# Optimization experiments

Measured on AMD Instinct MI355X. Metric: run time of the kernel, lower is better.

The kernel has to match this reference:

```python
import jax, jax.numpy as jnp
import numpy as np

EMB = 1024
NUM_HEADS = 16
KEY_SIZE = 64
HEAD_SIZE = 64
EPS = 1.1920929e-07  # torch RMSNorm default eps=None -> finfo(float32).eps


def setup_inputs() -> dict:
    key = jax.random.key(0)
    ks = jax.random.split(key, 6)
    B, S = 2, 2048
    qkv_out = 2 * KEY_SIZE * NUM_HEADS + HEAD_SIZE * NUM_HEADS  # 3072
    return {
        "embeddings": jax.random.normal(ks[0], (B, S, EMB), dtype=jnp.float32),
        "cos_buffer": jax.random.uniform(ks[1], (S, KEY_SIZE), dtype=jnp.float32),
        "sin_buffer": jax.random.uniform(ks[2], (S, KEY_SIZE), dtype=jnp.float32),
        "norm_weight": jnp.ones((EMB,), dtype=jnp.float32),
        "qkv_weight": jax.random.normal(ks[3], (qkv_out, EMB), dtype=jnp.float32) * (EMB ** -0.5),
        "out_weight": jax.random.normal(ks[4], (EMB, NUM_HEADS * HEAD_SIZE), dtype=jnp.float32) * ((NUM_HEADS * HEAD_SIZE) ** -0.5),
    }


def _rotate(feat, cos_b, sin_b):
    # feat: [B, H, S, key_size]; torch code: cat(second_half, first_half) (no negation)
    half = KEY_SIZE // 2
    swapped = jnp.concatenate((feat[..., half:], feat[..., :half]), axis=-1)
    return cos_b * feat + sin_b * swapped


def reference(embeddings, cos_buffer, sin_buffer, norm_weight, qkv_weight, out_weight):
    B, S, D = embeddings.shape
    # RMSNorm
    rms = jnp.sqrt(jnp.mean(embeddings * embeddings, axis=-1, keepdims=True) + EPS)
    normed = embeddings / rms * norm_weight
    # fused QKV projection (torch Linear: x @ W.T)
    qkv = normed @ qkv_weight.T  # [B, S, 3072]
    ks = KEY_SIZE * NUM_HEADS
    q = qkv[..., :ks].reshape(B, S, NUM_HEADS, KEY_SIZE).transpose(0, 2, 1, 3)
    k = qkv[..., ks:2 * ks].reshape(B, S, NUM_HEADS, KEY_SIZE).transpose(0, 2, 1, 3)
    v = qkv[..., 2 * ks:].reshape(B, S, NUM_HEADS, HEAD_SIZE).transpose(0, 2, 1, 3)
    q = _rotate(q, cos_buffer, sin_buffer)
    k = _rotate(k, cos_buffer, sin_buffer)
    # causal scaled dot product attention
    scale = 1.0 / jnp.sqrt(jnp.float32(KEY_SIZE))
    scores = jnp.einsum("bhqd,bhkd->bhqk", q, k) * scale  # [B,H,S,S]
    causal = jnp.tril(jnp.ones((S, S), dtype=bool))
    scores = jnp.where(causal, scores, jnp.float32(-jnp.inf))
    probs = jax.nn.softmax(scores, axis=-1)
    attn = jnp.einsum("bhqk,bhkd->bhqd", probs, v)  # [B,H,S,head]
    attn = attn.transpose(0, 2, 1, 3).reshape(B, S, NUM_HEADS * HEAD_SIZE)
    out = attn @ out_weight.T
    return embeddings + out
```

## Files before the change

### kernel.cpp

```cpp
#include <hip/hip_runtime.h>
#include <hip/hip_bf16.h>
#include <stdint.h>

#define EMB 1024
#define SEQ 2048
#define NB 2
#define NH 16
#define HD 64
#define QKVN 3072
#define BSROWS (NB*SEQ)

typedef __attribute__((ext_vector_type(8))) short short8;
typedef __attribute__((ext_vector_type(4))) float f32x4;
typedef __attribute__((ext_vector_type(4))) unsigned short u16x4;

__device__ __forceinline__ float bf2f(unsigned short u){
  union{uint32_t i; float f;} x; x.i = ((uint32_t)u)<<16; return x.f;
}
__device__ __forceinline__ unsigned short f2bf(float f){
  union{float f; uint32_t i;} x; x.f = f;
  return (unsigned short)((x.i + 0x7FFFu + ((x.i>>16)&1u))>>16);
}

__device__ __forceinline__ void gload_lds16(const void* g, void* l){
  __builtin_amdgcn_global_load_lds((const __attribute__((address_space(1))) void*)g,
                                   (__attribute__((address_space(3))) void*)l, 16, 0, 0);
}

__global__ __launch_bounds__(256) void k_rmsnorm(const float* __restrict__ x,
                                                 const float* __restrict__ w,
                                                 unsigned short* __restrict__ out){
  int row = blockIdx.x;
  const float4* xr = (const float4*)(x + (size_t)row*EMB);
  float4 v = xr[threadIdx.x];
  float ss = v.x*v.x + v.y*v.y + v.z*v.z + v.w*v.w;
  #pragma unroll
  for(int m=1;m<64;m<<=1) ss += __shfl_xor(ss, m, 64);
  __shared__ float red[4];
  if((threadIdx.x & 63)==0) red[threadIdx.x>>6] = ss;
  __syncthreads();
  float tot = red[0]+red[1]+red[2]+red[3];
  float rinv = rsqrtf(tot*(1.0f/EMB) + 1.1920929e-07f);
  float4 wv = ((const float4*)w)[threadIdx.x];
  u16x4 o;
  o.x = f2bf(v.x*wv.x*rinv); o.y = f2bf(v.y*wv.y*rinv);
  o.z = f2bf(v.z*wv.z*rinv); o.w = f2bf(v.w*wv.w*rinv);
  *(u16x4*)(out + (size_t)row*EMB + threadIdx.x*4) = o;
}

__global__ __launch_bounds__(256) void k_f2bf2(const float* __restrict__ a,
                                               const float* __restrict__ b,
                                               unsigned short* __restrict__ oa,
                                               unsigned short* __restrict__ ob,
                                               int na4, int nb4){
  int i = blockIdx.x*256 + threadIdx.x;
  const float* src; unsigned short* dst; int idx;
  if(i < na4){ src = a; dst = oa; idx = i; }
  else { idx = i - na4; if(idx >= nb4) return; src = b; dst = ob; }
  float4 v = ((const float4*)src)[idx];
  u16x4 o;
  o.x = f2bf(v.x); o.y = f2bf(v.y); o.z = f2bf(v.z); o.w = f2bf(v.w);
  ((u16x4*)dst)[idx] = o;
}

template<int MODE>
__global__ __launch_bounds__(256) void k_gemm(const unsigned short* __restrict__ A,
                                              const unsigned short* __restrict__ W,
                                              unsigned short* __restrict__ Cb,
                                              float* __restrict__ Cf,
                                              const float* __restrict__ resid,
                                              int M, int N, int K){
  __shared__ unsigned short As[128*64];
  __shared__ unsigned short Bs[128*64];
  const int tid = threadIdx.x;
  const int l  = tid & 63;
  const int wid = tid >> 6;
  const int lr = l & 15, lh = l >> 4;
  const int m0 = blockIdx.y * 128, n0 = blockIdx.x * 128;
  const int wr = wid >> 1, wc = wid & 1;
  const int swz = lr & 7;

  f32x4 acc[4][4] = {};

  const int nk = K >> 6;
  for(int kt=0; kt<nk; kt++){
    const int k0 = kt*64;
    #pragma unroll
    for(int j=0;j<4;j++){
      int c = j*256 + tid;
      int sb = j*256 + wid*64;
      int r = c >> 3, kc = c & 7;
      gload_lds16(A + (size_t)(m0+r)*K + k0 + ((kc ^ (r & 7))*8), &As[(size_t)sb*8]);
      gload_lds16(W + (size_t)(n0+r)*K + k0 + ((kc ^ (r & 7))*8), &Bs[(size_t)sb*8]);
    }
    __syncthreads();
    #pragma unroll
    for(int kk=0; kk<2; kk++){
      short8 af[4], bfr[4];
      #pragma unroll
      for(int i=0;i<4;i++){
        int ra = wr*64 + i*16 + lr;
        int rb = wc*64 + i*16 + lr;
        af[i]  = *(const short8*)&As[(size_t)((ra*8 + ((kk*4+lh) ^ swz))*8)];
        bfr[i] = *(const short8*)&Bs[(size_t)((rb*8 + ((kk*4+lh) ^ swz))*8)];
      }
      #pragma unroll
      for(int i=0;i<4;i++)
        #pragma unroll
        for(int jn=0;jn<4;jn++)
          acc[i][jn] = __builtin_amdgcn_mfma_f32_16x16x32_bf16(af[i], bfr[jn], acc[i][jn], 0,0,0);
    }
    __syncthreads();
  }

  const int rbase = m0 + wr*64, cbase = n0 + wc*64;
  #pragma unroll
  for(int i=0;i<4;i++){
    #pragma unroll
    for(int jn=0;jn<4;jn++){
      int rr = rbase + i*16 + lh*4;
      int cc = cbase + jn*16 + lr;
      #pragma unroll
      for(int t=0;t<4;t++){
        float val = acc[i][jn][t];
        if(MODE==0){
          Cb[(size_t)(rr+t)*N + cc] = f2bf(val);
        } else {
          Cf[(size_t)(rr+t)*N + cc] = val + resid[(size_t)(rr+t)*N + cc];
        }
      }
    }
  }
}

__global__ __launch_bounds__(256) void k_rope(const unsigned short* __restrict__ qkv,
                                              const float* __restrict__ cosb,
                                              const float* __restrict__ sinb,
                                              unsigned short* __restrict__ qb,
                                              unsigned short* __restrict__ kb){
  int t = blockIdx.x*256 + threadIdx.x;
  int g = t & 7;
  int h = (t >> 3) & 15;
  int part = (t >> 7) & 1;
  int r = t >> 8;
  int b = r >> 11, s = r & 2047;
  const float qs = part ? 1.0f : 0.125f*1.4426950408889634f;
  const unsigned short* src = qkv + (size_t)r*QKVN + part*1024 + h*64 + g*4;
  u16x4 xl = *(const u16x4*)src;
  u16x4 xh = *(const u16x4*)(src + 32);
  f32x4 cl = *(const f32x4*)(cosb + s*64 + g*4);
  f32x4 ch = *(const f32x4*)(cosb + s*64 + 32 + g*4);
  f32x4 sl = *(const f32x4*)(sinb + s*64 + g*4);
  f32x4 sh = *(const f32x4*)(sinb + s*64 + 32 + g*4);
  u16x4 lo, hi;
  #pragma unroll
  for(int j=0;j<4;j++){
    float a = bf2f(xl[j]), bb = bf2f(xh[j]);
    lo[j] = f2bf((cl[j]*a  + sl[j]*bb)*qs);
    hi[j] = f2bf((ch[j]*bb + sh[j]*a)*qs);
  }
  unsigned short* dst = (part ? kb : qb) + ((size_t)((b*NH + h)*SEQ + s))*HD + g*4;
  *(u16x4*)dst = lo;
  *(u16x4*)(dst + 32) = hi;
}

__global__ __launch_bounds__(256) void k_vt(const unsigned short* __restrict__ qkv,
                                            unsigned short* __restrict__ vt){
  __shared__ unsigned short t[64][65];
  int bh = blockIdx.y;
  int b = bh >> 4, h = bh & 15;
  int s0 = blockIdx.x*64;
  int tid = threadIdx.x;
  #pragma unroll
  for(int it=0; it<4; it++){
    int idx = it*256 + tid;
    int si = idx >> 4;
    int dj = (idx & 15)*4;
    const unsigned short* g = qkv + (size_t)(b*SEQ + s0 + si)*QKVN + 2048 + h*64 + dj;
    u16x4 v = *(const u16x4*)g;
    t[dj+0][si] = v.x; t[dj+1][si] = v.y; t[dj+2][si] = v.z; t[dj+3][si] = v.w;
  }
  __syncthreads();
  int d = tid >> 2, sc = (tid & 3)*16;
  unsigned short* out = vt + (size_t)(bh*64 + d)*SEQ + s0 + sc;
  #pragma unroll
  for(int u=0;u<4;u++){
    u16x4 o;
    #pragma unroll
    for(int e=0;e<4;e++){
      int n = sc + u*4 + e;
      int blk32 = n >> 5, n32 = n & 31;
      int nc = n32 >> 2, e4 = n32 & 3;
      int oc = (nc & 1) ? (4 + (nc >> 1)) : (nc >> 1);
      o[e] = t[d][blk32*32 + oc*4 + e4];
    }
    *(u16x4*)(out + u*4) = o;
  }
}

__global__ __launch_bounds__(256, 4) void k_attn(const unsigned short* __restrict__ Q,
                                                 const unsigned short* __restrict__ K,
                                                 const unsigned short* __restrict__ Vt,
                                                 unsigned short* __restrict__ O){
  __shared__ unsigned short Ks[2][64*64];
  __shared__ unsigned short Vs[2][64*64];
  const int tid = threadIdx.x;
  const int l = tid & 63, wid = tid >> 6;
  const int lr = l & 15, lh = l >> 4;
  const int id = blockIdx.x;
  const int bh = (id & 7)*4 + ((id >> 3) & 3);
  const int p  = id >> 5;
  const unsigned short* Kp = K + (size_t)bh*SEQ*HD;
  const unsigned short* Vp = Vt + (size_t)bh*HD*SEQ;
  const int b = bh >> 4, h = bh & 15;
  const int swz = lr & 7;

  #define STAGE(t_, b_) { \
    const int kv0s = (t_)*64; \
    _Pragma("unroll") \
    for(int j=0;j<2;j++){ \
      int s = j*256 + tid; \
      int sb = j*256 + wid*64; \
      int r = s >> 3, c = s & 7; \
      gload_lds16(Kp + (size_t)(kv0s + r)*HD + ((c ^ (r & 7))*8), &Ks[b_][sb*8]); \
      gload_lds16(Vp + (size_t)r*SEQ + kv0s + ((c ^ (r & 7))*8), &Vs[b_][sb*8]); \
    } }

  for(int pass = 0; pass < 2; pass++){
    const int qblk = pass ? p : (31 - p);
    const int q0 = qblk*64 + wid*16;
    const unsigned short* Qp = Q + ((size_t)bh*SEQ + q0)*HD;

    short8 qf0 = *(const short8*)&Qp[lr*HD + lh*8];
    short8 qf1 = *(const short8*)&Qp[lr*HD + 32 + lh*8];

    f32x4 o[4] = {};
    float m_ = -__builtin_inff();
    float ls = 0.f;
    const int qg = q0 + lr;
    const int T = qblk + 1;

    auto body = [&](int kv0, const unsigned short* Kb, const unsigned short* Vb,
                    bool masked){
      f32x4 s4[4] = {};
      #pragma unroll
      for(int i=0;i<4;i++){
        int row = i*16 + lr;
        short8 ka = *(const short8*)&Kb[(row*8 + (lh ^ swz))*8];
        short8 kc = *(const short8*)&Kb[(row*8 + ((4+lh) ^ swz))*8];
        s4[i] = __builtin_amdgcn_mfma_f32_16x16x32_bf16(ka, qf0, s4[i], 0,0,0);
        s4[i] = __builtin_amdgcn_mfma_f32_16x16x32_bf16(kc, qf1, s4[i], 0,0,0);
      }
      float v[16];
      #pragma unroll
      for(int i=0;i<4;i++)
        #pragma unroll
        for(int j=0;j<4;j++){
          float val = s4[i][j];
          if(masked){
            int kvg = kv0 + i*16 + lh*4 + j;
            val = (kvg <= qg) ? val : -__builtin_inff();
          }
          v[i*4+j] = val;
        }
      float pm = v[0];
      #pragma unroll
      for(int j=1;j<16;j++) pm = fmaxf(pm, v[j]);
      if(__any(pm > m_ + 11.544f)){
        float mx = fmaxf(pm, __shfl_xor(pm, 16, 64));
        mx = fmaxf(mx, __shfl_xor(mx, 32, 64));
        float mn = fmaxf(m_, mx);
        float cr = __builtin_amdgcn_exp2f(m_ - mn);
        m_ = mn;
        ls *= cr;
        #pragma unroll
        for(int f=0; f<4; f++) o[f] *= cr;
      }
      float pp[16], rs = 0.f;
      #pragma unroll
      for(int j=0;j<16;j++){ pp[j] = __builtin_amdgcn_exp2f(v[j] - m_); rs += pp[j]; }
      ls += rs;

      union { short8 s8; uint32_t u[4]; } P0, P1;
      #pragma unroll
      for(int j=0;j<4;j++){
        asm("v_cvt_pk_bf16_f32 %0, %1, %2" : "=v"(P0.u[j]) : "v"(pp[2*j]),   "v"(pp[2*j+1]));
        asm("v_cvt_pk_bf16_f32 %0, %1, %2" : "=v"(P1.u[j]) : "v"(pp[8+2*j]), "v"(pp[8+2*j+1]));
      }
      #pragma unroll
      for(int f=0; f<4; f++){
        int row = f*16 + lr;
        short8 va  = *(const short8*)&Vb[(row*8 + (lh ^ swz))*8];
        short8 vb2 = *(const short8*)&Vb[(row*8 + ((4+lh) ^ swz))*8];
        o[f] = __builtin_amdgcn_mfma_f32_16x16x32_bf16(va,  P0.s8, o[f], 0,0,0);
        o[f] = __builtin_amdgcn_mfma_f32_16x16x32_bf16(vb2, P1.s8, o[f], 0,0,0);
      }
    };

    STAGE(0, 0);
    __syncthreads();
    int cur = 0;

    for(int t = 0; t < T-1; t++){
      STAGE(t+1, cur^1);
      body(t*64, Ks[cur], Vs[cur], false);
      __syncthreads();
      cur ^= 1;
    }
    body((T-1)*64, Ks[cur], Vs[cur], true);

    ls += __shfl_xor(ls, 16, 64);
    ls += __shfl_xor(ls, 32, 64);

    const float inv = 1.0f/ls;
    #pragma unroll
    for(int f=0; f<4; f++){
      u16x4 ov;
      #pragma unroll
      for(int t2=0;t2<4;t2++) ov[t2] = f2bf(o[f][t2]*inv);
      *(u16x4*)&O[(size_t)(b*SEQ + qg)*EMB + h*HD + f*16 + lh*4] = ov;
    }
    __syncthreads();
  }
  #undef STAGE
}

extern "C" void kernel_launch(void* const* d_in, const int* in_sizes, int n_in,
                              void* d_out, int out_size, void* d_ws, size_t ws_size,
                              hipStream_t stream) {
  const float* emb   = (const float*)d_in[0];
  const float* cosb  = (const float*)d_in[1];
  const float* sinb  = (const float*)d_in[2];
  const float* nw    = (const float*)d_in[3];
  const float* qkvw  = (const float*)d_in[4];
  const float* outw  = (const float*)d_in[5];
  float* out = (float*)d_out;

  unsigned short* ws = (unsigned short*)d_ws;
  unsigned short* qkvWb = ws;
  unsigned short* outWb = qkvWb + (size_t)QKVN*EMB;
  unsigned short* normed = outWb + (size_t)EMB*EMB;
  unsigned short* attnout = normed;
  unsigned short* qkvb = normed + (size_t)BSROWS*EMB;
  unsigned short* qb = qkvb + (size_t)BSROWS*QKVN;
  unsigned short* kb = qb + (size_t)NB*NH*SEQ*HD;
  unsigned short* vtb = kb + (size_t)NB*NH*SEQ*HD;

  const int na4 = QKVN*EMB/4, nb4 = EMB*EMB/4;
  k_rmsnorm<<<dim3(BSROWS), dim3(256), 0, stream>>>(emb, nw, normed);
  k_f2bf2<<<dim3((na4+nb4+255)/256), dim3(256), 0, stream>>>(qkvw, outw, qkvWb, outWb, na4, nb4);
  k_gemm<0><<<dim3(QKVN/128, BSROWS/128), dim3(256), 0, stream>>>(
      normed, qkvWb, qkvb, nullptr, nullptr, BSROWS, QKVN, EMB);
  k_rope<<<dim3(BSROWS, 1), dim3(256), 0, stream>>>(qkvb, cosb, sinb, qb, kb);
  k_vt<<<dim3(SEQ/64, NB*NH), dim3(256), 0, stream>>>(qkvb, vtb);
  k_attn<<<dim3(512), dim3(256), 0, stream>>>(qb, kb, vtb, attnout);
  k_gemm<1><<<dim3(EMB/128, BSROWS/128), dim3(256), 0, stream>>>(
      attnout, outWb, nullptr, out, emb, BSROWS, EMB, EMB);
}
```

Measured before the change: 188.8 us.

## Triple-buffer LDS staging in GEMM and attention with vmcnt-based single barrier

```diff
diff --git a/kernel.cpp b/kernel.cpp
--- a/kernel.cpp
+++ b/kernel.cpp
@@ -70,48 +70,58 @@
                                               float* __restrict__ Cf,
                                               const float* __restrict__ resid,
                                               int M, int N, int K){
-  __shared__ unsigned short As[128*64];
-  __shared__ unsigned short Bs[128*64];
+  __shared__ unsigned short As[3*128*32];
+  __shared__ unsigned short Bs[3*128*32];
   const int tid = threadIdx.x;
   const int l  = tid & 63;
   const int wid = tid >> 6;
   const int lr = l & 15, lh = l >> 4;
   const int m0 = blockIdx.y * 128, n0 = blockIdx.x * 128;
   const int wr = wid >> 1, wc = wid & 1;
-  const int swz = lr & 7;
 
   f32x4 acc[4][4] = {};
-
-  const int nk = K >> 6;
-  for(int kt=0; kt<nk; kt++){
-    const int k0 = kt*64;
-    #pragma unroll
-    for(int j=0;j<4;j++){
-      int c = j*256 + tid;
-      int sb = j*256 + wid*64;
-      int r = c >> 3, kc = c & 7;
-      gload_lds16(A + (size_t)(m0+r)*K + k0 + ((kc ^ (r & 7))*8), &As[(size_t)sb*8]);
-      gload_lds16(W + (size_t)(n0+r)*K + k0 + ((kc ^ (r & 7))*8), &Bs[(size_t)sb*8]);
-    }
-    __syncthreads();
-    #pragma unroll
-    for(int kk=0; kk<2; kk++){
-      short8 af[4], bfr[4];
-      #pragma unroll
-      for(int i=0;i<4;i++){
-        int ra = wr*64 + i*16 + lr;
-        int rb = wc*64 + i*16 + lr;
-        af[i]  = *(const short8*)&As[(size_t)((ra*8 + ((kk*4+lh) ^ swz))*8)];
-        bfr[i] = *(const short8*)&Bs[(size_t)((rb*8 + ((kk*4+lh) ^ swz))*8)];
-      }
-      #pragma unroll
-      for(int i=0;i<4;i++)
-        #pragma unroll
-        for(int jn=0;jn<4;jn++)
-          acc[i][jn] = __builtin_amdgcn_mfma_f32_16x16x32_bf16(af[i], bfr[jn], acc[i][jn], 0,0,0);
-    }
-    __syncthreads();
-  }
+  const int nk = K >> 5;
+
+  #define GSTAGE(kt_, s_) { \
+    const int k0 = (kt_)*32; \
+    _Pragma("unroll") \
+    for(int j=0;j<2;j++){ \
+      int c = j*256 + tid; \
+      int sb = (s_)*512 + j*256 + wid*64; \
+      int r = c >> 2, kc = c & 3; \
+      gload_lds16(A + (size_t)(m0+r)*K + k0 + ((kc ^ ((r>>1)&3))*8), &As[(size_t)sb*8]); \
+      gload_lds16(W + (size_t)(n0+r)*K + k0 + ((kc ^ ((r>>1)&3))*8), &Bs[(size_t)sb*8]); \
+    } }
+
+  #define GCOMPUTE(s_) { \
+    short8 af[4], bfr[4]; \
+    _Pragma("unroll") \
+    for(int i=0;i<4;i++){ \
+      int ra = wr*64 + i*16 + lr, rb = wc*64 + i*16 + lr; \
+      af[i]  = *(const short8*)&As[(size_t)((s_)*512 + ra*4 + (lh ^ ((ra>>1)&3)))*8]; \
+      bfr[i] = *(const short8*)&Bs[(size_t)((s_)*512 + rb*4 + (lh ^ ((rb>>1)&3)))*8]; \
+    } \
+    _Pragma("unroll") \
+    for(int i=0;i<4;i++) \
+      _Pragma("unroll") \
+      for(int jn=0;jn<4;jn++) \
+        acc[i][jn] = __builtin_amdgcn_mfma_f32_16x16x32_bf16(af[i], bfr[jn], acc[i][jn], 0,0,0); \
+  }
+
+  GSTAGE(0, 0);
+  GSTAGE(1, 1);
+  int cur = 0, nxt = 2;
+  for(int kt = 0; kt < nk-1; kt++){
+    asm volatile("s_waitcnt vmcnt(4)\ns_barrier" ::: "memory");
+    if(kt + 2 < nk) GSTAGE(kt+2, nxt);
+    GCOMPUTE(cur);
+    cur = (cur==2) ? 0 : cur+1;
+    nxt = (nxt==2) ? 0 : nxt+1;
+  }
+  asm volatile("s_waitcnt vmcnt(0)\ns_barrier" ::: "memory");
+  GCOMPUTE(cur);
+  #undef GSTAGE
+  #undef GCOMPUTE
 
   const int rbase = m0 + wr*64, cbase = n0 + wc*64;
   #pragma unroll
@@ -202,8 +212,8 @@
                                                  const unsigned short* __restrict__ K,
                                                  const unsigned short* __restrict__ Vt,
                                                  unsigned short* __restrict__ O){
-  __shared__ unsigned short Ks[2][64*64];
-  __shared__ unsigned short Vs[2][64*64];
+  __shared__ unsigned short Ks[3][64*64];
+  __shared__ unsigned short Vs[3][64*64];
   const int tid = threadIdx.x;
   const int l = tid & 63, wid = tid >> 6;
   const int lr = l & 15, lh = l >> 4;
@@ -215,15 +225,15 @@
   const int b = bh >> 4, h = bh & 15;
   const int swz = lr & 7;
 
-  #define STAGE(t_, b_) { \
+  #define STAGE(t_, s_) { \
     const int kv0s = (t_)*64; \
     _Pragma("unroll") \
     for(int j=0;j<2;j++){ \
       int s = j*256 + tid; \
       int sb = j*256 + wid*64; \
       int r = s >> 3, c = s & 7; \
-      gload_lds16(Kp + (size_t)(kv0s + r)*HD + ((c ^ (r & 7))*8), &Ks[b_][sb*8]); \
-      gload_lds16(Vp + (size_t)r*SEQ + kv0s + ((c ^ (r & 7))*8), &Vs[b_][sb*8]); \
+      gload_lds16(Kp + (size_t)(kv0s + r)*HD + ((c ^ (r & 7))*8), &Ks[s_][sb*8]); \
+      gload_lds16(Vp + (size_t)r*SEQ + kv0s + ((c ^ (r & 7))*8), &Vs[s_][sb*8]); \
     } }
 
   for(int pass = 0; pass < 2; pass++){
@@ -298,15 +308,16 @@
     };
 
     STAGE(0, 0);
-    __syncthreads();
-    int cur = 0;
-
+    if(T > 1) STAGE(1, 1);
+    int cur = 0, nxt = 2;
     for(int t = 0; t < T-1; t++){
-      STAGE(t+1, cur^1);
+      asm volatile("s_waitcnt vmcnt(4)\ns_barrier" ::: "memory");
+      if(t + 2 < T) STAGE(t+2, nxt);
       body(t*64, Ks[cur], Vs[cur], false);
-      __syncthreads();
-      cur ^= 1;
+      cur = (cur==2) ? 0 : cur+1;
+      nxt = (nxt==2) ? 0 : nxt+1;
     }
+    asm volatile("s_waitcnt vmcnt(0)\ns_barrier" ::: "memory");
     body((T-1)*64, Ks[cur], Vs[cur], true);
 
     ls += __shfl_xor(ls, 16, 64);
```

New measurement: 194.1 us. 2.8% more time.
